# Performance work log

Measured on AMD Instinct MI355X. Metric: run time of the kernel, lower is better.

Reference implementation:

```python
import jax, jax.numpy as jnp
import numpy as np

N_NODES = 100000
N_EDGES = 3200000
N_GRAPHS = 1024
K = 32  # total number of kernels (num_kernel1..4 = 8 each)


def setup_inputs() -> dict:
    key = jax.random.key(0)
    ks = jax.random.split(key, 20)
    inp = {
        'x': jax.random.normal(ks[0], (N_NODES, 5), jnp.float32),
        'p': jax.random.normal(ks[1], (N_NODES, 3), jnp.float32),
        'edge_attr': jax.random.normal(ks[2], (N_EDGES, 1), jnp.float32),
        'Wx0': jax.random.normal(ks[3], (5, K), jnp.float32) * 0.3,
        'Wx1': jax.random.normal(ks[4], (K, K), jnp.float32) * 0.1,
        'Wx2': jax.random.normal(ks[5], (K, K), jnp.float32) * 0.1,
        'Wp0': jax.random.normal(ks[6], (3, K), jnp.float32) * 0.3,
        'Wp1': jax.random.normal(ks[7], (3, K), jnp.float32) * 0.3,
        'Wp2': jax.random.normal(ks[8], (3, K), jnp.float32) * 0.3,
        'We0': jax.random.normal(ks[9], (1, K), jnp.float32) * 0.3,
        'We1': jax.random.normal(ks[10], (1, K), jnp.float32) * 0.3,
        'We2': jax.random.normal(ks[11], (1, K), jnp.float32) * 0.3,
        'b0': jax.random.normal(ks[12], (K,), jnp.float32) * 0.1,
        'b1': jax.random.normal(ks[13], (K,), jnp.float32) * 0.1,
        'b2': jax.random.normal(ks[14], (K,), jnp.float32) * 0.1,
        'Wh': jax.random.normal(ks[15], (K, 1), jnp.float32) * 0.1,
        'bh': jax.random.normal(ks[16], (1,), jnp.float32) * 0.1,
        'edge_index': jax.random.randint(ks[17], (2, N_EDGES), 0, N_NODES, jnp.int64 if jax.config.jax_enable_x64 else jnp.int32),
        'batch': jnp.sort(jax.random.randint(ks[18], (N_NODES,), 0, N_GRAPHS, jnp.int64 if jax.config.jax_enable_x64 else jnp.int32)),
    }
    return inp


def _gnn_forward(x, p, edge_attr, Wxs, Wps, Wes, bs, edge_index):
    src, dst = edge_index[0], edge_index[1]
    p_rel = p[src] - p[dst]                      # [E, 3] relative positions
    h = x
    for Wx, Wp, We, b in zip(Wxs, Wps, Wes, bs):
        # kernel similarity per edge: gather neighbor feats + geometry, score vs K kernels
        msg = jnp.tanh(h[src] @ Wx + p_rel @ Wp + edge_attr @ We + b)   # [E, K]
        sim_sc = jax.ops.segment_sum(msg, dst, num_segments=N_NODES)    # [N, K] node sim scores
        # MolGCN.propagate: message(sim_sc_j) with aggr='add'
        h = jax.ops.segment_sum(sim_sc[src], dst, num_segments=N_NODES)  # [N, K]
    return h


def reference(x, p, edge_attr, Wx0, Wx1, Wx2, Wp0, Wp1, Wp2, We0, We1, We2,
              b0, b1, b2, Wh, bh, edge_index, batch):
    h = _gnn_forward(x, p, edge_attr, (Wx0, Wx1, Wx2), (Wp0, Wp1, Wp2),
                     (We0, We1, We2), (b0, b1, b2), edge_index)
    # global_mean_pool over graphs
    sums = jax.ops.segment_sum(h, batch, num_segments=N_GRAPHS)          # [G, K]
    cnt = jax.ops.segment_sum(jnp.ones((N_NODES,), h.dtype), batch, num_segments=N_GRAPHS)
    graph_rep = sums / jnp.maximum(cnt, 1.0)[:, None]                    # [G, K]
    pred = graph_rep @ Wh + bh                                           # [G, 1]
    return (pred, graph_rep)
```

## Files before the change

kernel.cpp:

```cpp
#include <hip/hip_runtime.h>
#include <hip/hip_fp16.h>

#define K_DIM 32
#define BN 256
#define MAXBUCK 512

__device__ __forceinline__ float tanh_fast(float x) {
    float e = exp2f(x * 2.8853901817f);
    return fmaf(-2.0f, __builtin_amdgcn_rcpf(e + 1.0f), 1.0f);
}


__global__ void k_bcnt(const int* __restrict__ dst, int* __restrict__ bcnt,
                       int E, int nbuck) {
    __shared__ int h[MAXBUCK];
    for (int i = threadIdx.x; i < nbuck; i += blockDim.x) h[i] = 0;
    __syncthreads();
    for (int e = blockIdx.x * blockDim.x + threadIdx.x; e < E; e += gridDim.x * blockDim.x)
        atomicAdd(&h[dst[e] >> 8], 1);
    __syncthreads();
    for (int i = threadIdx.x; i < nbuck; i += blockDim.x)
        if (h[i]) atomicAdd(&bcnt[i], h[i]);
}

__global__ void k_bscan(const int* __restrict__ bcnt, int* __restrict__ boff,
                        int* __restrict__ gcur, int nbuck, int total) {
    __shared__ int sm[256];
    __shared__ int carry;
    int t = threadIdx.x;
    if (t == 0) carry = 0;
    __syncthreads();
    for (int base = 0; base < nbuck; base += 256) {
        int v = (base + t < nbuck) ? bcnt[base + t] : 0;
        sm[t] = v;
        __syncthreads();
        #pragma unroll
        for (int d = 1; d < 256; d <<= 1) {
            int tv = (t >= d) ? sm[t - d] : 0;
            __syncthreads();
            sm[t] += tv;
            __syncthreads();
        }
        int excl = carry + sm[t] - v;
        if (base + t < nbuck) { boff[base + t] = excl; gcur[base + t] = excl; }
        __syncthreads();
        if (t == 0) carry += sm[255];
        __syncthreads();
    }
    if (t == 0) boff[nbuck] = total;
}

__global__ void k_bscatter(const int* __restrict__ src, const int* __restrict__ dst,
                           const float* __restrict__ ea, int* __restrict__ gcur,
                           uint2* __restrict__ rec, int E, int nbuck) {
    __shared__ int lcnt[MAXBUCK];
    __shared__ int lbase[MAXBUCK];
    const int nb = gridDim.x;
    const long c0 = (long)E * blockIdx.x / nb;
    const long c1 = (long)E * (blockIdx.x + 1) / nb;
    for (int i = threadIdx.x; i < nbuck; i += blockDim.x) lcnt[i] = 0;
    __syncthreads();
    for (long e = c0 + threadIdx.x; e < c1; e += blockDim.x)
        atomicAdd(&lcnt[dst[e] >> 8], 1);
    __syncthreads();
    for (int i = threadIdx.x; i < nbuck; i += blockDim.x) {
        int c = lcnt[i];
        lbase[i] = c ? atomicAdd(&gcur[i], c) : 0;
    }
    __syncthreads();
    for (int i = threadIdx.x; i < nbuck; i += blockDim.x) lcnt[i] = 0;
    __syncthreads();
    for (long e = c0 + threadIdx.x; e < c1; e += blockDim.x) {
        int d = dst[e];
        int b = d >> 8;
        int rank = atomicAdd(&lcnt[b], 1);
        unsigned meta = ((unsigned)(d & 255) << 17) | (unsigned)src[e];
        rec[lbase[b] + rank] = make_uint2(meta, __float_as_uint(ea[e]));
    }
}

__global__ void k_blocal(const uint2* __restrict__ rec, uint2* __restrict__ rec2,
                         int* __restrict__ srcs2, const int* __restrict__ boff,
                         int* __restrict__ off, int N, int E) {
    __shared__ int cnt[BN];
    __shared__ int base[BN];
    __shared__ int sm[BN];
    const int b = blockIdx.x;
    const int tid = threadIdx.x;
    int e0 = boff[b], e1 = boff[b + 1];
    int tot = e1 - e0;
    cnt[tid] = 0;
    __syncthreads();
    for (int i = tid; i < tot; i += 256)
        atomicAdd(&cnt[rec[e0 + i].x >> 17], 1);
    __syncthreads();
    int v = cnt[tid];
    sm[tid] = v;
    __syncthreads();
    #pragma unroll
    for (int d = 1; d < 256; d <<= 1) {
        int tv = (tid >= d) ? sm[tid - d] : 0;
        __syncthreads();
        sm[tid] += tv;
        __syncthreads();
    }
    base[tid] = sm[tid] - v;
    int n = b * BN + tid;
    if (n < N) off[n] = e0 + base[tid];
    if (b == 0 && tid == 0) off[N] = E;
    cnt[tid] = 0;
    __syncthreads();
    for (int i = tid; i < tot; i += 256) {
        uint2 r = rec[e0 + i];
        int dl = r.x >> 17;
        int rank = atomicAdd(&cnt[dl], 1);
        int pos = e0 + base[dl] + rank;
        unsigned s = r.x & 0x1FFFFu;
        rec2[pos] = make_uint2(s, r.y);
        srcs2[pos] = (int)s;
    }
}


__global__ void k_node_gemm5(const float* __restrict__ h, const float* __restrict__ p,
                             const float* __restrict__ Wx, const float* __restrict__ Wp,
                             __half* __restrict__ Mh, int n_nodes) {
    __shared__ float sWx[5 * 32];
    __shared__ float sWp[96];
    for (int i = threadIdx.x; i < 5 * 32; i += blockDim.x) sWx[i] = Wx[i];
    if (threadIdx.x < 96) sWp[threadIdx.x] = Wp[threadIdx.x];
    __syncthreads();
    const int k = threadIdx.x & 31;
    int n = blockIdx.x * (blockDim.x >> 5) + (threadIdx.x >> 5);
    if (n >= n_nodes) return;
    float hv = (k < 5) ? h[n * 5 + k] : 0.0f;
    float pv = (k < 3) ? p[n * 3 + k] : 0.0f;
    float acc = 0.0f;
    #pragma unroll
    for (int j = 0; j < 5; ++j) acc = fmaf(__shfl(hv, j, 32), sWx[j * 32 + k], acc);
    #pragma unroll
    for (int j = 0; j < 3; ++j) acc = fmaf(__shfl(pv, j, 32), sWp[j * 32 + k], acc);
    Mh[n * 32 + k] = __float2half(acc);
}

__global__ void k_edge_msg(const __half* __restrict__ Mh, const float* __restrict__ p,
                           const int* __restrict__ off, const uint2* __restrict__ rec,
                           const float* __restrict__ Wp, const float* __restrict__ We,
                           const float* __restrict__ b,
                           __half* __restrict__ simh, int N) {
    __shared__ uint2 stage[8][32];
    const int k = threadIdx.x & 31;
    const int grp = threadIdx.x >> 5;
    int n = blockIdx.x * 8 + grp;
    if (n >= N) return;

    float pn = (k < 3) ? p[n * 3 + k] : 0.0f;
    float cnst = b[k] - (__shfl(pn, 0, 32) * Wp[k] + __shfl(pn, 1, 32) * Wp[32 + k]
                         + __shfl(pn, 2, 32) * Wp[64 + k]);
    float we = We[k];
    float acc = 0.0f;

    int e0 = off[n], e1 = off[n + 1];
    for (int base = e0; base < e1; base += 32) {
        int m = min(32, e1 - base);
        uint2 r = (k < m) ? rec[base + k] : make_uint2(0u, 0u);
        stage[grp][k] = r;
        for (int j = 0; j < m; j += 16) {
            float mv[16], av[16];
            #pragma unroll
            for (int u = 0; u < 16; ++u) {
                uint2 e = stage[grp][j + u];
                av[u] = __uint_as_float(e.y);
                mv[u] = __half2float(Mh[e.x * 32 + k]);
            }
            #pragma unroll
            for (int u = 0; u < 16; ++u)
                if (j + u < m) acc += tanh_fast(fmaf(av[u], we, cnst) + mv[u]);
        }
    }
    simh[n * 32 + k] = __float2half(acc);
}

template <int FUSE>
__global__ void k_prop_gemm(const __half* __restrict__ simh, const int* __restrict__ off,
                            const int* __restrict__ srcs, const float* __restrict__ p,
                            const float* __restrict__ Wx, const float* __restrict__ Wp,
                            __half* __restrict__ outMh, float* __restrict__ outF,
                            int N) {
    __shared__ float sWx[1024];
    __shared__ int stageS[8][32];
    if (FUSE) {
        for (int i = threadIdx.x; i < 1024; i += blockDim.x) sWx[i] = Wx[i];
        __syncthreads();
    }
    const int k = threadIdx.x & 31;
    const int grp = threadIdx.x >> 5;
    int n = blockIdx.x * 8 + grp;
    if (n >= N) return;

    float acc = 0.0f;
    int e0 = off[n], e1 = off[n + 1];
    for (int base = e0; base < e1; base += 32) {
        int m = min(32, e1 - base);
        int sv = (k < m) ? srcs[base + k] : 0;
        stageS[grp][k] = sv;
        for (int j = 0; j < m; j += 16) {
            float t[16];
            #pragma unroll
            for (int u = 0; u < 16; ++u) {
                int s = stageS[grp][j + u];
                t[u] = __half2float(simh[s * 32 + k]);
            }
            #pragma unroll
            for (int u = 0; u < 16; ++u)
                if (j + u < m) acc += t[u];
        }
    }

    if (!FUSE) { outF[n * 32 + k] = acc; return; }
    float mm = 0.0f;
    #pragma unroll
    for (int j = 0; j < 32; ++j) mm = fmaf(__shfl(acc, j, 32), sWx[j * 32 + k], mm);
    float pv = (k < 3) ? p[n * 3 + k] : 0.0f;
    mm = fmaf(__shfl(pv, 0, 32), Wp[k], mm);
    mm = fmaf(__shfl(pv, 1, 32), Wp[32 + k], mm);
    mm = fmaf(__shfl(pv, 2, 32), Wp[64 + k], mm);
    outMh[n * 32 + k] = __float2half(mm);
}


__global__ void k_pool(const float* __restrict__ h, const int* __restrict__ batch,
                       const float* __restrict__ Wh, const float* __restrict__ bh,
                       float* __restrict__ out, int n_nodes, int n_graphs) {
    __shared__ int sLo, sHi;
    __shared__ float red[256];
    int g = blockIdx.x;
    if (threadIdx.x == 0) {
        int lo = 0, hi = n_nodes;
        while (lo < hi) { int m = (lo + hi) >> 1; if (batch[m] < g) lo = m + 1; else hi = m; }
        sLo = lo;
        lo = 0; hi = n_nodes; int g1 = g + 1;
        while (lo < hi) { int m = (lo + hi) >> 1; if (batch[m] < g1) lo = m + 1; else hi = m; }
        sHi = lo;
    }
    __syncthreads();
    int lo = sLo, hi = sHi;
    int k = threadIdx.x & 31, r = threadIdx.x >> 5;
    float acc = 0.0f;
    for (int n = lo + r; n < hi; n += 8) acc += h[n * 32 + k];
    red[threadIdx.x] = acc;
    __syncthreads();
    if (threadIdx.x < 32) {
        float s = 0.0f;
        #pragma unroll
        for (int r2 = 0; r2 < 8; ++r2) s += red[r2 * 32 + k];
        float c = (float)(hi - lo);
        float rep = s / fmaxf(c, 1.0f);
        out[n_graphs + g * 32 + k] = rep;
        float t = rep * Wh[k];
        #pragma unroll
        for (int d = 16; d > 0; d >>= 1) t += __shfl_down(t, d, 32);
        if (k == 0) out[g] = t + bh[0];
    }
}


extern "C" void kernel_launch(void* const* d_in, const int* in_sizes, int n_in,
                              void* d_out, int out_size, void* d_ws, size_t ws_size,
                              hipStream_t stream) {
    const float* x   = (const float*)d_in[0];
    const float* p   = (const float*)d_in[1];
    const float* ea  = (const float*)d_in[2];
    const float* Wx0 = (const float*)d_in[3];
    const float* Wx1 = (const float*)d_in[4];
    const float* Wx2 = (const float*)d_in[5];
    const float* Wp0 = (const float*)d_in[6];
    const float* Wp1 = (const float*)d_in[7];
    const float* Wp2 = (const float*)d_in[8];
    const float* We0 = (const float*)d_in[9];
    const float* We1 = (const float*)d_in[10];
    const float* We2 = (const float*)d_in[11];
    const float* b0  = (const float*)d_in[12];
    const float* b1  = (const float*)d_in[13];
    const float* b2  = (const float*)d_in[14];
    const float* Wh  = (const float*)d_in[15];
    const float* bh  = (const float*)d_in[16];
    const int* edge_index = (const int*)d_in[17];
    const int* batch      = (const int*)d_in[18];

    const int N = in_sizes[0] / 5;
    const int E = in_sizes[17] / 2;
    const int G = out_size / 33;
    const int nbuck = (N + BN - 1) / BN;

    const int* srcp = edge_index;
    const int* dstp = edge_index + E;

    char* w = (char*)d_ws;
    auto alloc = [&](size_t bytes) -> void* {
        void* r = (void*)w;
        w += (bytes + 255) & ~(size_t)255;
        return r;
    };
    int*    bcnt  = (int*)alloc((size_t)nbuck * 4);
    int*    boff  = (int*)alloc((size_t)(nbuck + 1) * 4);
    int*    gcur  = (int*)alloc((size_t)nbuck * 4);
    int*    off   = (int*)alloc((size_t)(N + 1) * 4);
    uint2*  rec   = (uint2*)alloc((size_t)E * 8);
    uint2*  rec2  = (uint2*)alloc((size_t)E * 8);
    int*    srcs2 = (int*)alloc((size_t)E * 4);
    __half* Mh    = (__half*)alloc((size_t)N * K_DIM * 2);
    __half* simh  = (__half*)alloc((size_t)N * K_DIM * 2);
    float*  hB    = (float*)alloc((size_t)N * K_DIM * 4);

    (void)hipMemsetAsync(bcnt, 0, (size_t)nbuck * 4, stream);
    k_bcnt<<<1024, 256, 0, stream>>>(dstp, bcnt, E, nbuck);
    k_bscan<<<1, 256, 0, stream>>>(bcnt, boff, gcur, nbuck, E);
    k_bscatter<<<256, 1024, 0, stream>>>(srcp, dstp, ea, gcur, rec, E, nbuck);
    k_blocal<<<nbuck, 256, 0, stream>>>(rec, rec2, srcs2, boff, off, N, E);

    const int NB = (N + 7) / 8;

    k_node_gemm5<<<NB, 256, 0, stream>>>(x, p, Wx0, Wp0, Mh, N);
    k_edge_msg<<<NB, 256, 0, stream>>>(Mh, p, off, rec2, Wp0, We0, b0, simh, N);
    k_prop_gemm<1><<<NB, 256, 0, stream>>>(simh, off, srcs2, p, Wx1, Wp1, Mh, nullptr, N);
    k_edge_msg<<<NB, 256, 0, stream>>>(Mh, p, off, rec2, Wp1, We1, b1, simh, N);
    k_prop_gemm<1><<<NB, 256, 0, stream>>>(simh, off, srcs2, p, Wx2, Wp2, Mh, nullptr, N);
    k_edge_msg<<<NB, 256, 0, stream>>>(Mh, p, off, rec2, Wp2, We2, b2, simh, N);
    k_prop_gemm<0><<<NB, 256, 0, stream>>>(simh, off, srcs2, p, nullptr, nullptr, nullptr, hB, N);

    k_pool<<<G, 256, 0, stream>>>(hB, batch, Wh, bh, (float*)d_out, N, G);
}
```

Baseline: 462.5 us.

## Use packed half2 math for edge tanh messages and half2 gathers

The edge message kernel now processes two channels per lane in packed half2 arithmetic, with each half-wave handling alternate edges. The tanh scale factor is folded into the node GEMM weights, biases and edge weights. Edge attributes are pre-converted to duplicated half2, and tanh is rewritten as deg - 2*sum(1/(exp2+1)). The propagation kernel likewise gathers half2 pairs and reduces across the two half-waves. This roughly halves ALU and gather instruction count but lowers precision to fp16 inside the exp/rcp and the per-chunk accumulation.

```diff
diff --git a/kernel.cpp b/kernel.cpp
--- a/kernel.cpp
+++ b/kernel.cpp
@@ -4,11 +4,7 @@
 #define K_DIM 32
 #define BN 256
 #define MAXBUCK 512
-
-__device__ __forceinline__ float tanh_fast(float x) {
-    float e = exp2f(x * 2.8853901817f);
-    return fmaf(-2.0f, __builtin_amdgcn_rcpf(e + 1.0f), 1.0f);
-}
+#define TANH_SCALE 2.8853900817779268f
 
 
 __global__ void k_bcnt(const int* __restrict__ dst, int* __restrict__ bcnt,
@@ -116,7 +112,10 @@
         int rank = atomicAdd(&cnt[dl], 1);
         int pos = e0 + base[dl] + rank;
         unsigned s = r.x & 0x1FFFFu;
-        rec2[pos] = make_uint2(s, r.y);
+        float eaf = __uint_as_float(r.y);
+        __half eh = __float2half(eaf);
+        unsigned hb = (unsigned)__half_as_ushort(eh);
+        rec2[pos] = make_uint2(s, (hb << 16) | hb);
         srcs2[pos] = (int)s;
     }
 }
@@ -127,8 +126,8 @@
                              __half* __restrict__ Mh, int n_nodes) {
     __shared__ float sWx[5 * 32];
     __shared__ float sWp[96];
-    for (int i = threadIdx.x; i < 5 * 32; i += blockDim.x) sWx[i] = Wx[i];
-    if (threadIdx.x < 96) sWp[threadIdx.x] = Wp[threadIdx.x];
+    for (int i = threadIdx.x; i < 5 * 32; i += blockDim.x) sWx[i] = Wx[i] * TANH_SCALE;
+    if (threadIdx.x < 96) sWp[threadIdx.x] = Wp[threadIdx.x] * TANH_SCALE;
     __syncthreads();
     const int k = threadIdx.x & 31;
     int n = blockIdx.x * (blockDim.x >> 5) + (threadIdx.x >> 5);
@@ -146,39 +145,66 @@
 __global__ void k_edge_msg(const __half* __restrict__ Mh, const float* __restrict__ p,
                            const int* __restrict__ off, const uint2* __restrict__ rec,
                            const float* __restrict__ Wp, const float* __restrict__ We,
-                           const float* __restrict__ b,
+                           const float* __restrict__ bias,
                            __half* __restrict__ simh, int N) {
     __shared__ uint2 stage[8][32];
-    const int k = threadIdx.x & 31;
+    const int l = threadIdx.x & 31;
+    const int c = l & 15;
+    const int q = l >> 4;
     const int grp = threadIdx.x >> 5;
     int n = blockIdx.x * 8 + grp;
     if (n >= N) return;
 
-    float pn = (k < 3) ? p[n * 3 + k] : 0.0f;
-    float cnst = b[k] - (__shfl(pn, 0, 32) * Wp[k] + __shfl(pn, 1, 32) * Wp[32 + k]
-                         + __shfl(pn, 2, 32) * Wp[64 + k]);
-    float we = We[k];
-    float acc = 0.0f;
-
+    const __half2* Mh2 = (const __half2*)Mh;
+
+    float2 wef = ((const float2*)We)[c];
+    __half2 we2 = __floats2half2_rn(wef.x * TANH_SCALE, wef.y * TANH_SCALE);
+    float2 b2  = ((const float2*)bias)[c];
+    float2 wp0 = ((const float2*)Wp)[c];
+    float2 wp1 = ((const float2*)(Wp + 32))[c];
+    float2 wp2 = ((const float2*)(Wp + 64))[c];
+    float pn = (l < 3) ? p[n * 3 + l] : 0.0f;
+    float pn0 = __shfl(pn, 0, 32), pn1 = __shfl(pn, 1, 32), pn2 = __shfl(pn, 2, 32);
+    __half2 cnst2 = __floats2half2_rn(
+        (b2.x - (pn0 * wp0.x + pn1 * wp1.x + pn2 * wp2.x)) * TANH_SCALE,
+        (b2.y - (pn0 * wp0.y + pn1 * wp1.y + pn2 * wp2.y)) * TANH_SCALE);
+    const __half2 one2  = __floats2half2_rn(1.0f, 1.0f);
+    const __half2 zero2 = __floats2half2_rn(0.0f, 0.0f);
+
+    float fx = 0.0f, fy = 0.0f;
     int e0 = off[n], e1 = off[n + 1];
     for (int base = e0; base < e1; base += 32) {
         int m = min(32, e1 - base);
-        uint2 r = (k < m) ? rec[base + k] : make_uint2(0u, 0u);
-        stage[grp][k] = r;
+        uint2 r = (l < m) ? rec[base + l] : make_uint2(0u, 0u);
+        stage[grp][l] = r;
+        __half2 acc2 = zero2;
         for (int j = 0; j < m; j += 16) {
-            float mv[16], av[16];
+            __half2 mv[8], av[8];
             #pragma unroll
-            for (int u = 0; u < 16; ++u) {
-                uint2 e = stage[grp][j + u];
-                av[u] = __uint_as_float(e.y);
-                mv[u] = __half2float(Mh[e.x * 32 + k]);
+            for (int u = 0; u < 8; ++u) {
+                uint2 e = stage[grp][j + 2 * u + q];
+                unsigned eb = e.y;
+                av[u] = *(const __half2*)&eb;
+                mv[u] = Mh2[e.x * 16 + c];
             }
             #pragma unroll
-            for (int u = 0; u < 16; ++u)
-                if (j + u < m) acc += tanh_fast(fmaf(av[u], we, cnst) + mv[u]);
+            for (int u = 0; u < 8; ++u) {
+                __half2 arg = __hadd2(__hfma2(av[u], we2, cnst2), mv[u]);
+                __half2 ex  = h2exp2(arg);
+                __half2 rr  = h2rcp(__hadd2(ex, one2));
+                rr = (j + 2 * u + q < m) ? rr : zero2;
+                acc2 = __hadd2(acc2, rr);
+            }
         }
-    }
-    simh[n * 32 + k] = __float2half(acc);
+        fx += __low2float(acc2);
+        fy += __high2float(acc2);
+    }
+    fx += __shfl_xor(fx, 16, 32);
+    fy += __shfl_xor(fy, 16, 32);
+    float deg = (float)(e1 - e0);
+    if (l < 16)
+        ((__half2*)simh)[n * 16 + c] =
+            __floats2half2_rn(fmaf(-2.0f, fx, deg), fmaf(-2.0f, fy, deg));
 }
 
 template <int FUSE>
@@ -190,42 +216,58 @@
     __shared__ float sWx[1024];
     __shared__ int stageS[8][32];
     if (FUSE) {
-        for (int i = threadIdx.x; i < 1024; i += blockDim.x) sWx[i] = Wx[i];
-        __syncthreads();
-    }
-    const int k = threadIdx.x & 31;
+        for (int i = threadIdx.x; i < 1024; i += blockDim.x) sWx[i] = Wx[i] * TANH_SCALE;
+        __syncthreads();
+    }
+    const int l = threadIdx.x & 31;
+    const int c = l & 15;
+    const int q = l >> 4;
     const int grp = threadIdx.x >> 5;
     int n = blockIdx.x * 8 + grp;
     if (n >= N) return;
 
-    float acc = 0.0f;
+    const __half2* sim2 = (const __half2*)simh;
+    const __half2 zero2 = __floats2half2_rn(0.0f, 0.0f);
+    float fx = 0.0f, fy = 0.0f;
     int e0 = off[n], e1 = off[n + 1];
     for (int base = e0; base < e1; base += 32) {
         int m = min(32, e1 - base);
-        int sv = (k < m) ? srcs[base + k] : 0;
-        stageS[grp][k] = sv;
+        stageS[grp][l] = (l < m) ? srcs[base + l] : 0;
         for (int j = 0; j < m; j += 16) {
-            float t[16];
+            __half2 v[8];
             #pragma unroll
-            for (int u = 0; u < 16; ++u) {
-                int s = stageS[grp][j + u];
-                t[u] = __half2float(simh[s * 32 + k]);
+            for (int u = 0; u < 8; ++u) {
+                int s = stageS[grp][j + 2 * u + q];
+                v[u] = sim2[s * 16 + c];
             }
             #pragma unroll
-            for (int u = 0; u < 16; ++u)
-                if (j + u < m) acc += t[u];
+            for (int u = 0; u < 8; ++u) {
+                __half2 vz = (j + 2 * u + q < m) ? v[u] : zero2;
+                fx += __low2float(vz);
+                fy += __high2float(vz);
+            }
         }
     }
-
-    if (!FUSE) { outF[n * 32 + k] = acc; return; }
+    fx += __shfl_xor(fx, 16, 32);
+    fy += __shfl_xor(fy, 16, 32);
+
+    if (!FUSE) {
+        if (l < 16) ((float2*)outF)[n * 16 + c] = make_float2(fx, fy);
+        return;
+    }
     float mm = 0.0f;
     #pragma unroll
-    for (int j = 0; j < 32; ++j) mm = fmaf(__shfl(acc, j, 32), sWx[j * 32 + k], mm);
-    float pv = (k < 3) ? p[n * 3 + k] : 0.0f;
-    mm = fmaf(__shfl(pv, 0, 32), Wp[k], mm);
-    mm = fmaf(__shfl(pv, 1, 32), Wp[32 + k], mm);
-    mm = fmaf(__shfl(pv, 2, 32), Wp[64 + k], mm);
-    outMh[n * 32 + k] = __float2half(mm);
+    for (int i = 0; i < 16; ++i) {
+        float hx = __shfl(fx, i, 32);
+        float hy = __shfl(fy, i, 32);
+        mm = fmaf(hx, sWx[(2 * i) * 32 + l], mm);
+        mm = fmaf(hy, sWx[(2 * i + 1) * 32 + l], mm);
+    }
+    float pv = (l < 3) ? p[n * 3 + l] : 0.0f;
+    float pp = __shfl(pv, 0, 32) * Wp[l] + __shfl(pv, 1, 32) * Wp[32 + l]
+             + __shfl(pv, 2, 32) * Wp[64 + l];
+    mm = fmaf(pp, TANH_SCALE, mm);
+    outMh[n * 32 + l] = __float2half(mm);
 }
 
 
```

Result: faster. 432.6 us (-6.5%).
